# Performance work log

Hardware: AMD Instinct MI355X
Metric: run time of the kernel (lower is better)

Reference implementation:

```python
import jax, jax.numpy as jnp
from jax import lax
import numpy as np

H = 51  # hidden size hardcoded in the module


def setup_inputs() -> dict:
    key = jax.random.key(0)
    ks = jax.random.split(key, 12)
    B, T = 4096, 256
    s_in = 1.0 / np.sqrt(H)
    inp = {
        "input": jax.random.normal(ks[0], (B, T), dtype=jnp.float32),
        # LSTMCell 1: input dim 1 -> hidden 51 (gates stacked i,f,g,o)
        "W_ih1": jax.random.uniform(ks[1], (4 * H, 1), jnp.float32, -s_in, s_in),
        "W_hh1": jax.random.uniform(ks[2], (4 * H, H), jnp.float32, -s_in, s_in),
        "b_ih1": jax.random.uniform(ks[3], (4 * H,), jnp.float32, -s_in, s_in),
        "b_hh1": jax.random.uniform(ks[4], (4 * H,), jnp.float32, -s_in, s_in),
        # LSTMCell 2: hidden 51 -> hidden 51
        "W_ih2": jax.random.uniform(ks[5], (4 * H, H), jnp.float32, -s_in, s_in),
        "W_hh2": jax.random.uniform(ks[6], (4 * H, H), jnp.float32, -s_in, s_in),
        "b_ih2": jax.random.uniform(ks[7], (4 * H,), jnp.float32, -s_in, s_in),
        "b_hh2": jax.random.uniform(ks[8], (4 * H,), jnp.float32, -s_in, s_in),
        # Linear head 51 -> 1
        "W_lin": jax.random.uniform(ks[9], (1, H), jnp.float32, -s_in, s_in),
        "b_lin": jax.random.uniform(ks[10], (1,), jnp.float32, -s_in, s_in),
    }
    return inp


def _lstm_cell(x_t, h, c, W_ih, W_hh, b_ih, b_hh):
    # PyTorch LSTMCell: gates = x W_ih^T + b_ih + h W_hh^T + b_hh, order i,f,g,o
    g = x_t @ W_ih.T + b_ih + h @ W_hh.T + b_hh  # [B, 4H]
    i, f, gg, o = jnp.split(g, 4, axis=-1)
    c_new = jax.nn.sigmoid(f) * c + jax.nn.sigmoid(i) * jnp.tanh(gg)
    h_new = jax.nn.sigmoid(o) * jnp.tanh(c_new)
    return h_new, c_new


def reference(input, W_ih1, W_hh1, b_ih1, b_hh1, W_ih2, W_hh2, b_ih2, b_hh2, W_lin, b_lin):
    B = input.shape[0]
    xs = input.T[:, :, None]  # [T, B, 1] -- one scalar feature per timestep

    def step(carry, x_t):
        h1, c1, h2, c2 = carry
        h1, c1 = _lstm_cell(x_t, h1, c1, W_ih1, W_hh1, b_ih1, b_hh1)
        h2, c2 = _lstm_cell(h1, h2, c2, W_ih2, W_hh2, b_ih2, b_hh2)
        out = h2 @ W_lin.T + b_lin  # [B, 1]
        return (h1, c1, h2, c2), out

    z = jnp.zeros((B, H), dtype=input.dtype)
    _, outs = lax.scan(step, (z, z, z, z), xs)  # outs: [T, B, 1]
    # torch.stack(outputs, 1).squeeze(2) -> [B, T]
    return outs[:, :, 0].T
```

## Files before the change

### kernel.cpp

```cpp
#include <hip/hip_runtime.h>

#define HH 51
#define TT 256
#define NB 16
#define L2E 1.442695041f

typedef __attribute__((ext_vector_type(8))) _Float16 half8;
typedef __attribute__((ext_vector_type(4))) float   floatx4;

#define MFMA16F(A,B,C) __builtin_amdgcn_mfma_f32_16x16x32_f16((A),(B),(C),0,0,0)

__device__ __forceinline__ float rcp_fast(float x) { return __builtin_amdgcn_rcpf(x); }
#if __has_builtin(__builtin_amdgcn_exp2f)
__device__ __forceinline__ float exp2_fast(float x) { return __builtin_amdgcn_exp2f(x); }
#else
__device__ __forceinline__ float exp2_fast(float x) { return __expf(0.69314718056f * x); }
#endif
__device__ __forceinline__ unsigned short f2h_bits(float v) {
    return __builtin_bit_cast(unsigned short, (_Float16)v);
}

__global__ void lstm_prep(const float* __restrict__ Whh1, const float* __restrict__ Wih1,
                          const float* __restrict__ bih1, const float* __restrict__ bhh1,
                          const float* __restrict__ Wih2, const float* __restrict__ Whh2,
                          const float* __restrict__ bih2, const float* __restrict__ bhh2,
                          const float* __restrict__ Wlin, const float* __restrict__ blin,
                          uint4* __restrict__ frags) {
    int tid = blockIdx.x * blockDim.x + threadIdx.x;
    if (tid >= 196 * 64) return;
    int f = tid >> 6, lane = tid & 63;
    int n = lane & 15, qq = lane >> 4;
    int hl, s, tau, cell;
    if (f < 64)       { cell = 1; int r = f;       hl = r & 1; r >>= 1; s = r & 1; tau = r >> 1; }
    else if (f < 192) { cell = 2; int r = f - 64;  hl = r & 1; r >>= 1; s = r & 3; tau = r >> 2; }
    else              { cell = 3; int r = f - 192; hl = r & 1; s = r >> 1; tau = 0; }
    int g = tau >> 2, U = tau & 3, u = U * 16 + n;
    float sc = (cell == 3) ? 1.0f : ((g == 2) ? 2.0f * L2E : L2E);
    unsigned int dw[4];
    for (int d = 0; d < 4; d++) {
        unsigned int packed = 0;
        for (int e = 0; e < 2; e++) {
            int jj = d * 2 + e;
            int k = s * 32 + qq * 8 + jj;
            float val = 0.f;
            if (cell == 1) {
                if (u < HH) {
                    if (k < HH)       val = Whh1[(g * HH + u) * HH + k];
                    else if (k == 51) val = bih1[g * HH + u] + bhh1[g * HH + u];
                    else              val = Wih1[g * HH + u];
                }
            } else if (cell == 2) {
                if (u < HH) {
                    if (k < 64) {
                        if (k < HH)       val = Wih2[(g * HH + u) * HH + k];
                        else if (k == 51) val = bih2[g * HH + u] + bhh2[g * HH + u];
                    } else {
                        int k2 = k - 64;
                        if (k2 < HH) val = Whh2[(g * HH + u) * HH + k2];
                    }
                }
            } else {
                if (n == 0) {
                    if (k < HH)       val = Wlin[k];
                    else if (k == 51) val = blin[0];
                }
            }
            val *= sc;
            _Float16 hi = (_Float16)val;
            unsigned short bits;
            if (hl) { float lo = val - (float)hi; bits = f2h_bits(lo); }
            else    { bits = __builtin_bit_cast(unsigned short, hi); }
            packed |= ((unsigned int)bits) << (16 * e);
        }
        dw[d] = packed;
    }
    frags[f * 64 + lane] = make_uint4(dw[0], dw[1], dw[2], dw[3]);
}

__launch_bounds__(512, 2)
__global__ void lstm_main(const float* __restrict__ input,
                          const uint4* __restrict__ frags,
                          float* __restrict__ out) {
    __shared__ __align__(16) unsigned int h1[2][16][36];
    __shared__ __align__(16) unsigned int h2[2][16][36];
    __shared__ __align__(16) float xb[(TT + 1) * 16];

    const int tid  = threadIdx.x;
    const int lane = tid & 63;
    const int w    = tid >> 6;
    const int l15  = lane & 15;
    const int q    = lane >> 4;
    const int b0g  = blockIdx.x * NB;
    const bool c2w = (w < 4);
    const int U    = c2w ? w : (w - 4);
    const int uc   = U * 16 + l15;
    const bool uok = (uc < HH);

    for (int i = tid; i < 2 * 16 * 36; i += 512) {
        ((unsigned*)h1)[i] = 0; ((unsigned*)h2)[i] = 0;
    }
    for (int c = 0; c < 2; c++) {
        int flat = tid + c * 512;
        int b = flat >> 6, t0 = (flat & 63) * 4;
        float4 v = *(const float4*)&input[(size_t)(b0g + b) * TT + t0];
        xb[(t0 + 0) * 16 + b] = v.x; xb[(t0 + 1) * 16 + b] = v.y;
        xb[(t0 + 2) * 16 + b] = v.z; xb[(t0 + 3) * 16 + b] = v.w;
    }
    if (tid < 16) xb[TT * 16 + tid] = 0.f;
    __syncthreads();
    if (tid < 16) {
        int b = tid;
        int wi51 = ((25 + 4 * (b >> 1)) & 31) * 2 + 1;
        int wi52 = ((26 + 4 * (b >> 1)) & 31) * 2 + 0;
        int wi53 = ((26 + 4 * (b >> 1)) & 31) * 2 + 1;
        ((unsigned short*)&h1[1][b][0])[wi51] = 0x3C00;
        float x0 = input[(size_t)(b0g + b) * TT];
        _Float16 xh = (_Float16)x0;
        ((unsigned short*)&h1[1][b][0])[wi52] = __builtin_bit_cast(unsigned short, xh);
        ((unsigned short*)&h1[1][b][0])[wi53] = f2h_bits(x0 - (float)xh);
    }

    half8 fr[32];
    if (c2w) {
#pragma unroll
        for (int g = 0; g < 4; g++) {
            int tau = g * 4 + U;
#pragma unroll
            for (int s = 0; s < 4; s++) {
                fr[g * 8 + s * 2 + 0] = __builtin_bit_cast(half8, frags[(64 + (tau * 4 + s) * 2 + 0) * 64 + lane]);
                fr[g * 8 + s * 2 + 1] = __builtin_bit_cast(half8, frags[(64 + (tau * 4 + s) * 2 + 1) * 64 + lane]);
            }
        }
    } else {
#pragma unroll
        for (int g = 0; g < 4; g++) {
            int tau = g * 4 + U;
#pragma unroll
            for (int s = 0; s < 2; s++) {
                fr[g * 4 + s * 2 + 0] = __builtin_bit_cast(half8, frags[((tau * 2 + s) * 2 + 0) * 64 + lane]);
                fr[g * 4 + s * 2 + 1] = __builtin_bit_cast(half8, frags[((tau * 2 + s) * 2 + 1) * 64 + lane]);
            }
        }
#pragma unroll
        for (int s = 0; s < 2; s++) {
            fr[16 + s * 2 + 0] = __builtin_bit_cast(half8, frags[(192 + s * 2 + 0) * 64 + lane]);
            fr[16 + s * 2 + 1] = __builtin_bit_cast(half8, frags[(192 + s * 2 + 1) * 64 + lane]);
        }
    }
    floatx4 zacc = {0.f, 0.f, 0.f, 0.f};
    float cst[4] = {0.f, 0.f, 0.f, 0.f};
    const int baseA = (q * 4 + 4 * (l15 >> 1)) & 31;
    const int baseB = (baseA + 16) & 31;

    __syncthreads();

#define GTAIL(DG, FG, SGN)                                                      \
    _Pragma("unroll")                                                           \
    for (int r = 0; r < 4; r++) {                                               \
        float e = exp2_fast(SGN (DG)[r]);                                       \
        (FG)[r] = rcp_fast(1.0f + e);                                           \
    }

#define STEP(IT, P)                                                             \
    do {                                                                        \
        if (c2w) {                                                              \
            if ((IT) >= 1 && (IT) <= TT) {               \
                half8 a0 = *(const half8*)&h1[1 - (P)][l15][baseA];             \
                half8 a1 = *(const half8*)&h1[1 - (P)][l15][baseB];             \
                half8 a2 = *(const half8*)&h2[(P)][l15][baseA];                 \
                half8 a3 = *(const half8*)&h2[(P)][l15][baseB];                 \
                floatx4 d0, d1, d2, d3;                                         \
                d0 = MFMA16F(a0, fr[0],  zacc); d0 = MFMA16F(a0, fr[1],  d0);   \
                d1 = MFMA16F(a0, fr[8],  zacc); d1 = MFMA16F(a0, fr[9],  d1);   \
                d2 = MFMA16F(a0, fr[16], zacc); d2 = MFMA16F(a0, fr[17], d2);   \
                d3 = MFMA16F(a0, fr[24], zacc); d3 = MFMA16F(a0, fr[25], d3);   \
                d0 = MFMA16F(a1, fr[2],  d0);   d0 = MFMA16F(a1, fr[3],  d0);   \
                d1 = MFMA16F(a1, fr[10], d1);   d1 = MFMA16F(a1, fr[11], d1);   \
                d2 = MFMA16F(a1, fr[18], d2);   d2 = MFMA16F(a1, fr[19], d2);   \
                d3 = MFMA16F(a1, fr[26], d3);   d3 = MFMA16F(a1, fr[27], d3);   \
                d0 = MFMA16F(a2, fr[4],  d0);   d0 = MFMA16F(a2, fr[5],  d0);   \
                d1 = MFMA16F(a2, fr[12], d1);   d1 = MFMA16F(a2, fr[13], d1);   \
                d2 = MFMA16F(a2, fr[20], d2);   d2 = MFMA16F(a2, fr[21], d2);   \
                d3 = MFMA16F(a2, fr[28], d3);   d3 = MFMA16F(a2, fr[29], d3);   \
                d0 = MFMA16F(a3, fr[6],  d0);   d0 = MFMA16F(a3, fr[7],  d0);   \
                d1 = MFMA16F(a3, fr[14], d1);   d1 = MFMA16F(a3, fr[15], d1);   \
                d2 = MFMA16F(a3, fr[22], d2);   d2 = MFMA16F(a3, fr[23], d2);   \
                d3 = MFMA16F(a3, fr[30], d3);   d3 = MFMA16F(a3, fr[31], d3);   \
                floatx4 f0, f1, f2, f3;                                         \
                GTAIL(d0, f0, -) GTAIL(d1, f1, -) GTAIL(d2, f2, +) GTAIL(d3, f3, -) \
                _Pragma("unroll")                                               \
                for (int r = 0; r < 4; r++) {                                   \
                    float tgs = fmaf(-4.0f * L2E, f2[r], 2.0f * L2E);           \
                    float cn  = fmaf(f1[r], cst[r], f0[r] * tgs);               \
                    cst[r] = cn;                                                \
                    float th = fmaf(-2.0f, rcp_fast(1.0f + exp2_fast(cn)), 1.0f); \
                    float hv = f3[r] * th;                                      \
                    hv = uok ? hv : (uc == 51 ? 1.0f : 0.f);                    \
                    int bb = q * 4 + r;                                         \
                    int wi = (((uc >> 1) + 4 * (bb >> 1)) & 31) * 2 + (uc & 1); \
                    ((unsigned short*)&h2[1 - (P)][bb][0])[wi] = f2h_bits(hv);  \
                }                                                               \
            }                                                                   \
        } else {                                                                \
            if ((IT) <= TT - 1) {                          \
                float4 xn = {0.f, 0.f, 0.f, 0.f};                               \
                if (uc >= HH) xn = *(const float4*)&xb[((IT) + 1) * 16 + q * 4]; \
                half8 a0 = *(const half8*)&h1[1 - (P)][l15][baseA];             \
                half8 a1 = *(const half8*)&h1[1 - (P)][l15][baseB];             \
                floatx4 d0, d1, d2, d3;                                         \
                d0 = MFMA16F(a0, fr[0],  zacc); d0 = MFMA16F(a0, fr[1],  d0);   \
                d1 = MFMA16F(a0, fr[4],  zacc); d1 = MFMA16F(a0, fr[5],  d1);   \
                d2 = MFMA16F(a0, fr[8],  zacc); d2 = MFMA16F(a0, fr[9],  d2);   \
                d3 = MFMA16F(a0, fr[12], zacc); d3 = MFMA16F(a0, fr[13], d3);   \
                d0 = MFMA16F(a1, fr[2],  d0);   d0 = MFMA16F(a1, fr[3],  d0);   \
                d1 = MFMA16F(a1, fr[6],  d1);   d1 = MFMA16F(a1, fr[7],  d1);   \
                d2 = MFMA16F(a1, fr[10], d2);   d2 = MFMA16F(a1, fr[11], d2);   \
                d3 = MFMA16F(a1, fr[14], d3);   d3 = MFMA16F(a1, fr[15], d3);   \
                floatx4 f0, f1, f2, f3;                                         \
                GTAIL(d0, f0, -) GTAIL(d1, f1, -) GTAIL(d2, f2, +) GTAIL(d3, f3, -) \
                _Pragma("unroll")                                               \
                for (int r = 0; r < 4; r++) {                                   \
                    float tgs = fmaf(-4.0f * L2E, f2[r], 2.0f * L2E);           \
                    float cn  = fmaf(f1[r], cst[r], f0[r] * tgs);               \
                    cst[r] = cn;                                                \
                    float th = fmaf(-2.0f, rcp_fast(1.0f + exp2_fast(cn)), 1.0f); \
                    float hv = f3[r] * th;                                      \
                    hv = uok ? hv                                               \
                             : (uc == 51 ? 1.0f                                 \
                             : (uc == 52 ? xn[r]                                \
                             : (uc == 53 ? xn[r] - (float)(_Float16)xn[r] : 0.f))); \
                    int bb = q * 4 + r;                                         \
                    int wi = (((uc >> 1) + 4 * (bb >> 1)) & 31) * 2 + (uc & 1); \
                    ((unsigned short*)&h1[(P)][bb][0])[wi] = f2h_bits(hv);      \
                }                                                               \
            }                                                                   \
            if ((IT) >= 2 && (w - 4) == ((IT) & 3)) {         \
                half8 a2 = *(const half8*)&h2[(P)][l15][baseA];                 \
                half8 a3 = *(const half8*)&h2[(P)][l15][baseB];                 \
                floatx4 ho;                                                     \
                ho = MFMA16F(a2, fr[16], zacc); ho = MFMA16F(a2, fr[17], ho);   \
                ho = MFMA16F(a3, fr[18], ho);   ho = MFMA16F(a3, fr[19], ho);   \
                if (l15 == 0) {                                                 \
                    _Pragma("unroll")                                           \
                    for (int r = 0; r < 4; r++)                                 \
                        out[(size_t)(b0g + q * 4 + r) * TT + ((IT) - 2)] = ho[r]; \
                }                                                               \
            }                                                                   \
        }                                                                       \
        __syncthreads();                                                        \
    } while (0)

    for (int itp = 0; itp < TT + 2; itp += 2) {
        STEP(itp, 0);
        STEP(itp + 1, 1);
    }
#undef STEP
#undef GTAIL
}

extern "C" void kernel_launch(void* const* d_in, const int* in_sizes, int n_in,
                              void* d_out, int out_size, void* d_ws, size_t ws_size,
                              hipStream_t stream) {
    const float* input = (const float*)d_in[0];
    const float* Wih1  = (const float*)d_in[1];
    const float* Whh1  = (const float*)d_in[2];
    const float* bih1  = (const float*)d_in[3];
    const float* bhh1  = (const float*)d_in[4];
    const float* Wih2  = (const float*)d_in[5];
    const float* Whh2  = (const float*)d_in[6];
    const float* bih2  = (const float*)d_in[7];
    const float* bhh2  = (const float*)d_in[8];
    const float* Wlin  = (const float*)d_in[9];
    const float* blin  = (const float*)d_in[10];

    uint4* frags = (uint4*)d_ws;
    int B = in_sizes[0] / TT;

    lstm_prep<<<49, 256, 0, stream>>>(Whh1, Wih1, bih1, bhh1, Wih2, Whh2,
                                      bih2, bhh2, Wlin, blin, frags);
    lstm_main<<<B / NB, 512, 0, stream>>>(input, frags, (float*)d_out);
}
```

Before: 379.0 us.

## Replace block-wide barriers with LDS counter flags and 4-deep h ring buffers

Replaces the per-step __syncthreads lockstep between layer-1 and layer-2 wavegroups with producer/consumer counters in shared memory, using atomic release/acquire and s_sleep spin-waits. Hidden-state buffers grow from double to quadruple buffering, so layer-1 waves can run up to a few steps ahead of layer-2 waves. The aim is to remove full-workgroup barrier stalls and let the two layers' work overlap. The cost is spin-wait polling overhead, and correctness now rests on the ring depth and the counter targets.

New measurement: 386.8 us. +2.1%, slower.

```diff
diff --git a/kernel.cpp b/kernel.cpp
--- a/kernel.cpp
+++ b/kernel.cpp
@@ -77,13 +77,24 @@
     frags[f * 64 + lane] = make_uint4(dw[0], dw[1], dw[2], dw[3]);
 }
 
+__device__ __forceinline__ void wait_ge(int* c, int tgt) {
+    if (__hip_atomic_load(c, __ATOMIC_ACQUIRE, __HIP_MEMORY_SCOPE_WORKGROUP) >= tgt) return;
+    do { __builtin_amdgcn_s_sleep(1); }
+    while (__hip_atomic_load(c, __ATOMIC_ACQUIRE, __HIP_MEMORY_SCOPE_WORKGROUP) < tgt);
+}
+__device__ __forceinline__ void publish(int* c) {
+    if ((threadIdx.x & 63) == 0)
+        (void)__hip_atomic_fetch_add(c, 1, __ATOMIC_RELEASE, __HIP_MEMORY_SCOPE_WORKGROUP);
+}
+
 __launch_bounds__(512, 2)
 __global__ void lstm_main(const float* __restrict__ input,
                           const uint4* __restrict__ frags,
                           float* __restrict__ out) {
-    __shared__ __align__(16) unsigned int h1[2][16][36];
-    __shared__ __align__(16) unsigned int h2[2][16][36];
+    __shared__ __align__(16) unsigned int h1r[4][16][36];
+    __shared__ __align__(16) unsigned int h2r[4][16][36];
     __shared__ __align__(16) float xb[(TT + 1) * 16];
+    __shared__ int cnt1, cnt2;
 
     const int tid  = threadIdx.x;
     const int lane = tid & 63;
@@ -96,8 +107,8 @@
     const int uc   = U * 16 + l15;
     const bool uok = (uc < HH);
 
-    for (int i = tid; i < 2 * 16 * 36; i += 512) {
-        ((unsigned*)h1)[i] = 0; ((unsigned*)h2)[i] = 0;
+    for (int i = tid; i < 4 * 16 * 36; i += 512) {
+        ((unsigned*)h1r)[i] = 0; ((unsigned*)h2r)[i] = 0;
     }
     for (int c = 0; c < 2; c++) {
         int flat = tid + c * 512;
@@ -107,17 +118,18 @@
         xb[(t0 + 2) * 16 + b] = v.z; xb[(t0 + 3) * 16 + b] = v.w;
     }
     if (tid < 16) xb[TT * 16 + tid] = 0.f;
+    if (tid == 0) { cnt1 = 0; cnt2 = 0; }
     __syncthreads();
     if (tid < 16) {
         int b = tid;
         int wi51 = ((25 + 4 * (b >> 1)) & 31) * 2 + 1;
         int wi52 = ((26 + 4 * (b >> 1)) & 31) * 2 + 0;
         int wi53 = ((26 + 4 * (b >> 1)) & 31) * 2 + 1;
-        ((unsigned short*)&h1[1][b][0])[wi51] = 0x3C00;
+        ((unsigned short*)&h1r[3][b][0])[wi51] = 0x3C00;
         float x0 = input[(size_t)(b0g + b) * TT];
         _Float16 xh = (_Float16)x0;
-        ((unsigned short*)&h1[1][b][0])[wi52] = __builtin_bit_cast(unsigned short, xh);
-        ((unsigned short*)&h1[1][b][0])[wi53] = f2h_bits(x0 - (float)xh);
+        ((unsigned short*)&h1r[3][b][0])[wi52] = __builtin_bit_cast(unsigned short, xh);
+        ((unsigned short*)&h1r[3][b][0])[wi53] = f2h_bits(x0 - (float)xh);
     }
 
     half8 fr[32];
@@ -161,100 +173,102 @@
         (FG)[r] = rcp_fast(1.0f + e);                                           \
     }
 
-#define STEP(IT, P)                                                             \
-    do {                                                                        \
-        if (c2w) {                                                              \
-            if ((IT) >= 1 && (IT) <= TT) {               \
-                half8 a0 = *(const half8*)&h1[1 - (P)][l15][baseA];             \
-                half8 a1 = *(const half8*)&h1[1 - (P)][l15][baseB];             \
-                half8 a2 = *(const half8*)&h2[(P)][l15][baseA];                 \
-                half8 a3 = *(const half8*)&h2[(P)][l15][baseB];                 \
-                floatx4 d0, d1, d2, d3;                                         \
-                d0 = MFMA16F(a0, fr[0],  zacc); d0 = MFMA16F(a0, fr[1],  d0);   \
-                d1 = MFMA16F(a0, fr[8],  zacc); d1 = MFMA16F(a0, fr[9],  d1);   \
-                d2 = MFMA16F(a0, fr[16], zacc); d2 = MFMA16F(a0, fr[17], d2);   \
-                d3 = MFMA16F(a0, fr[24], zacc); d3 = MFMA16F(a0, fr[25], d3);   \
-                d0 = MFMA16F(a1, fr[2],  d0);   d0 = MFMA16F(a1, fr[3],  d0);   \
-                d1 = MFMA16F(a1, fr[10], d1);   d1 = MFMA16F(a1, fr[11], d1);   \
-                d2 = MFMA16F(a1, fr[18], d2);   d2 = MFMA16F(a1, fr[19], d2);   \
-                d3 = MFMA16F(a1, fr[26], d3);   d3 = MFMA16F(a1, fr[27], d3);   \
-                d0 = MFMA16F(a2, fr[4],  d0);   d0 = MFMA16F(a2, fr[5],  d0);   \
-                d1 = MFMA16F(a2, fr[12], d1);   d1 = MFMA16F(a2, fr[13], d1);   \
-                d2 = MFMA16F(a2, fr[20], d2);   d2 = MFMA16F(a2, fr[21], d2);   \
-                d3 = MFMA16F(a2, fr[28], d3);   d3 = MFMA16F(a2, fr[29], d3);   \
-                d0 = MFMA16F(a3, fr[6],  d0);   d0 = MFMA16F(a3, fr[7],  d0);   \
-                d1 = MFMA16F(a3, fr[14], d1);   d1 = MFMA16F(a3, fr[15], d1);   \
-                d2 = MFMA16F(a3, fr[22], d2);   d2 = MFMA16F(a3, fr[23], d2);   \
-                d3 = MFMA16F(a3, fr[30], d3);   d3 = MFMA16F(a3, fr[31], d3);   \
-                floatx4 f0, f1, f2, f3;                                         \
-                GTAIL(d0, f0, -) GTAIL(d1, f1, -) GTAIL(d2, f2, +) GTAIL(d3, f3, -) \
-                _Pragma("unroll")                                               \
-                for (int r = 0; r < 4; r++) {                                   \
-                    float tgs = fmaf(-4.0f * L2E, f2[r], 2.0f * L2E);           \
-                    float cn  = fmaf(f1[r], cst[r], f0[r] * tgs);               \
-                    cst[r] = cn;                                                \
-                    float th = fmaf(-2.0f, rcp_fast(1.0f + exp2_fast(cn)), 1.0f); \
-                    float hv = f3[r] * th;                                      \
-                    hv = uok ? hv : (uc == 51 ? 1.0f : 0.f);                    \
-                    int bb = q * 4 + r;                                         \
-                    int wi = (((uc >> 1) + 4 * (bb >> 1)) & 31) * 2 + (uc & 1); \
-                    ((unsigned short*)&h2[1 - (P)][bb][0])[wi] = f2h_bits(hv);  \
-                }                                                               \
-            }                                                                   \
-        } else {                                                                \
-            if ((IT) <= TT - 1) {                          \
-                float4 xn = {0.f, 0.f, 0.f, 0.f};                               \
-                if (uc >= HH) xn = *(const float4*)&xb[((IT) + 1) * 16 + q * 4]; \
-                half8 a0 = *(const half8*)&h1[1 - (P)][l15][baseA];             \
-                half8 a1 = *(const half8*)&h1[1 - (P)][l15][baseB];             \
-                floatx4 d0, d1, d2, d3;                                         \
-                d0 = MFMA16F(a0, fr[0],  zacc); d0 = MFMA16F(a0, fr[1],  d0);   \
-                d1 = MFMA16F(a0, fr[4],  zacc); d1 = MFMA16F(a0, fr[5],  d1);   \
-                d2 = MFMA16F(a0, fr[8],  zacc); d2 = MFMA16F(a0, fr[9],  d2);   \
-                d3 = MFMA16F(a0, fr[12], zacc); d3 = MFMA16F(a0, fr[13], d3);   \
-                d0 = MFMA16F(a1, fr[2],  d0);   d0 = MFMA16F(a1, fr[3],  d0);   \
-                d1 = MFMA16F(a1, fr[6],  d1);   d1 = MFMA16F(a1, fr[7],  d1);   \
-                d2 = MFMA16F(a1, fr[10], d2);   d2 = MFMA16F(a1, fr[11], d2);   \
-                d3 = MFMA16F(a1, fr[14], d3);   d3 = MFMA16F(a1, fr[15], d3);   \
-                floatx4 f0, f1, f2, f3;                                         \
-                GTAIL(d0, f0, -) GTAIL(d1, f1, -) GTAIL(d2, f2, +) GTAIL(d3, f3, -) \
-                _Pragma("unroll")                                               \
-                for (int r = 0; r < 4; r++) {                                   \
-                    float tgs = fmaf(-4.0f * L2E, f2[r], 2.0f * L2E);           \
-                    float cn  = fmaf(f1[r], cst[r], f0[r] * tgs);               \
-                    cst[r] = cn;                                                \
-                    float th = fmaf(-2.0f, rcp_fast(1.0f + exp2_fast(cn)), 1.0f); \
-                    float hv = f3[r] * th;                                      \
-                    hv = uok ? hv                                               \
-                             : (uc == 51 ? 1.0f                                 \
-                             : (uc == 52 ? xn[r]                                \
-                             : (uc == 53 ? xn[r] - (float)(_Float16)xn[r] : 0.f))); \
-                    int bb = q * 4 + r;                                         \
-                    int wi = (((uc >> 1) + 4 * (bb >> 1)) & 31) * 2 + (uc & 1); \
-                    ((unsigned short*)&h1[(P)][bb][0])[wi] = f2h_bits(hv);      \
-                }                                                               \
-            }                                                                   \
-            if ((IT) >= 2 && (w - 4) == ((IT) & 3)) {         \
-                half8 a2 = *(const half8*)&h2[(P)][l15][baseA];                 \
-                half8 a3 = *(const half8*)&h2[(P)][l15][baseB];                 \
-                floatx4 ho;                                                     \
-                ho = MFMA16F(a2, fr[16], zacc); ho = MFMA16F(a2, fr[17], ho);   \
-                ho = MFMA16F(a3, fr[18], ho);   ho = MFMA16F(a3, fr[19], ho);   \
-                if (l15 == 0) {                                                 \
-                    _Pragma("unroll")                                           \
-                    for (int r = 0; r < 4; r++)                                 \
-                        out[(size_t)(b0g + q * 4 + r) * TT + ((IT) - 2)] = ho[r]; \
-                }                                                               \
-            }                                                                   \
-        }                                                                       \
-        __syncthreads();                                                        \
-    } while (0)
-
-    for (int itp = 0; itp < TT + 2; itp += 2) {
-        STEP(itp, 0);
-        STEP(itp + 1, 1);
-    }
-#undef STEP
+    if (c2w) {
+        for (int s = 0; s < TT; ++s) {
+            wait_ge(&cnt2, 4 * s);
+            wait_ge(&cnt1, 4 * (s + 1));
+            const unsigned int* p1 = &h1r[s & 3][l15][0];
+            const unsigned int* p2 = &h2r[(s + 3) & 3][l15][0];
+            half8 a0 = *(const half8*)(p1 + baseA);
+            half8 a1 = *(const half8*)(p1 + baseB);
+            half8 a2 = *(const half8*)(p2 + baseA);
+            half8 a3 = *(const half8*)(p2 + baseB);
+            floatx4 d0, d1, d2, d3;
+            d0 = MFMA16F(a0, fr[0],  zacc); d0 = MFMA16F(a0, fr[1],  d0);
+            d1 = MFMA16F(a0, fr[8],  zacc); d1 = MFMA16F(a0, fr[9],  d1);
+            d2 = MFMA16F(a0, fr[16], zacc); d2 = MFMA16F(a0, fr[17], d2);
+            d3 = MFMA16F(a0, fr[24], zacc); d3 = MFMA16F(a0, fr[25], d3);
+            d0 = MFMA16F(a1, fr[2],  d0);   d0 = MFMA16F(a1, fr[3],  d0);
+            d1 = MFMA16F(a1, fr[10], d1);   d1 = MFMA16F(a1, fr[11], d1);
+            d2 = MFMA16F(a1, fr[18], d2);   d2 = MFMA16F(a1, fr[19], d2);
+            d3 = MFMA16F(a1, fr[26], d3);   d3 = MFMA16F(a1, fr[27], d3);
+            d0 = MFMA16F(a2, fr[4],  d0);   d0 = MFMA16F(a2, fr[5],  d0);
+            d1 = MFMA16F(a2, fr[12], d1);   d1 = MFMA16F(a2, fr[13], d1);
+            d2 = MFMA16F(a2, fr[20], d2);   d2 = MFMA16F(a2, fr[21], d2);
+            d3 = MFMA16F(a2, fr[28], d3);   d3 = MFMA16F(a2, fr[29], d3);
+            d0 = MFMA16F(a3, fr[6],  d0);   d0 = MFMA16F(a3, fr[7],  d0);
+            d1 = MFMA16F(a3, fr[14], d1);   d1 = MFMA16F(a3, fr[15], d1);
+            d2 = MFMA16F(a3, fr[22], d2);   d2 = MFMA16F(a3, fr[23], d2);
+            d3 = MFMA16F(a3, fr[30], d3);   d3 = MFMA16F(a3, fr[31], d3);
+            floatx4 f0, f1, f2, f3;
+            GTAIL(d0, f0, -) GTAIL(d1, f1, -) GTAIL(d2, f2, +) GTAIL(d3, f3, -)
+#pragma unroll
+            for (int r = 0; r < 4; r++) {
+                float tgs = fmaf(-4.0f * L2E, f2[r], 2.0f * L2E);
+                float cn  = fmaf(f1[r], cst[r], f0[r] * tgs);
+                cst[r] = cn;
+                float th = fmaf(-2.0f, rcp_fast(1.0f + exp2_fast(cn)), 1.0f);
+                float hv = f3[r] * th;
+                hv = uok ? hv : (uc == 51 ? 1.0f : 0.f);
+                int bb = q * 4 + r;
+                int wi = (((uc >> 1) + 4 * (bb >> 1)) & 31) * 2 + (uc & 1);
+                ((unsigned short*)&h2r[s & 3][bb][0])[wi] = f2h_bits(hv);
+            }
+            publish(&cnt2);
+        }
+    } else {
+        for (int t = 0; t < TT + 4; ++t) {
+            wait_ge(&cnt1, 4 * t);
+            if (t >= 4) wait_ge(&cnt2, 4 * (t - 3));
+            if (t >= 4 && U == (t & 3)) {
+                const unsigned int* p2 = &h2r[t & 3][l15][0];
+                half8 a2 = *(const half8*)(p2 + baseA);
+                half8 a3 = *(const half8*)(p2 + baseB);
+                floatx4 ho;
+                ho = MFMA16F(a2, fr[16], zacc); ho = MFMA16F(a2, fr[17], ho);
+                ho = MFMA16F(a3, fr[18], ho);   ho = MFMA16F(a3, fr[19], ho);
+                if (l15 == 0) {
+#pragma unroll
+                    for (int r = 0; r < 4; r++)
+                        out[(size_t)(b0g + q * 4 + r) * TT + (t - 4)] = ho[r];
+                }
+            }
+            if (t < TT) {
+                float4 xn = {0.f, 0.f, 0.f, 0.f};
+                if (uc >= HH) xn = *(const float4*)&xb[(t + 1) * 16 + q * 4];
+                const unsigned int* p1 = &h1r[(t + 3) & 3][l15][0];
+                half8 a0 = *(const half8*)(p1 + baseA);
+                half8 a1 = *(const half8*)(p1 + baseB);
+                floatx4 d0, d1, d2, d3;
+                d0 = MFMA16F(a0, fr[0],  zacc); d0 = MFMA16F(a0, fr[1],  d0);
+                d1 = MFMA16F(a0, fr[4],  zacc); d1 = MFMA16F(a0, fr[5],  d1);
+                d2 = MFMA16F(a0, fr[8],  zacc); d2 = MFMA16F(a0, fr[9],  d2);
+                d3 = MFMA16F(a0, fr[12], zacc); d3 = MFMA16F(a0, fr[13], d3);
+                d0 = MFMA16F(a1, fr[2],  d0);   d0 = MFMA16F(a1, fr[3],  d0);
+                d1 = MFMA16F(a1, fr[6],  d1);   d1 = MFMA16F(a1, fr[7],  d1);
+                d2 = MFMA16F(a1, fr[10], d2);   d2 = MFMA16F(a1, fr[11], d2);
+                d3 = MFMA16F(a1, fr[14], d3);   d3 = MFMA16F(a1, fr[15], d3);
+                floatx4 f0, f1, f2, f3;
+                GTAIL(d0, f0, -) GTAIL(d1, f1, -) GTAIL(d2, f2, +) GTAIL(d3, f3, -)
+#pragma unroll
+                for (int r = 0; r < 4; r++) {
+                    float tgs = fmaf(-4.0f * L2E, f2[r], 2.0f * L2E);
+                    float cn  = fmaf(f1[r], cst[r], f0[r] * tgs);
+                    cst[r] = cn;
+                    float th = fmaf(-2.0f, rcp_fast(1.0f + exp2_fast(cn)), 1.0f);
+                    float hv = f3[r] * th;
+                    hv = uok ? hv
+                             : (uc == 51 ? 1.0f
+                             : (uc == 52 ? xn[r]
+                             : (uc == 53 ? xn[r] - (float)(_Float16)xn[r] : 0.f)));
+                    int bb = q * 4 + r;
+                    int wi = (((uc >> 1) + 4 * (bb >> 1)) & 31) * 2 + (uc & 1);
+                    ((unsigned short*)&h1r[t & 3][bb][0])[wi] = f2h_bits(hv);
+                }
+            }
+            publish(&cnt1);
+        }
+    }
 #undef GTAIL
 }
 
```

## Merge cell1 and cell2 wave roles so each wave computes both layers

Applied to the files above, without the earlier changes.

The block shrinks from 8 waves, where 4 handled layer 1 and 4 handled layer 2 plus the output head, to 4 waves. Each wave now computes its slice of both LSTM cells and the linear head every step, and holds all weight fragments in registers. The aim is to fill the MFMA pipeline and reuse the shared-memory h1 loads across both cells, cutting per-step barrier cost and idle waves. In exchange, each wave holds more registers (52 half8 fragments) and does about twice the serial work per step, with fewer waves per CU to hide latency.

After: 466.2 us. 23.0% more time.

```diff
diff --git a/kernel.cpp b/kernel.cpp
--- a/kernel.cpp
+++ b/kernel.cpp
@@ -77,7 +77,7 @@
     frags[f * 64 + lane] = make_uint4(dw[0], dw[1], dw[2], dw[3]);
 }
 
-__launch_bounds__(512, 2)
+__launch_bounds__(256, 1)
 __global__ void lstm_main(const float* __restrict__ input,
                           const uint4* __restrict__ frags,
                           float* __restrict__ out) {
@@ -91,16 +91,14 @@
     const int l15  = lane & 15;
     const int q    = lane >> 4;
     const int b0g  = blockIdx.x * NB;
-    const bool c2w = (w < 4);
-    const int U    = c2w ? w : (w - 4);
-    const int uc   = U * 16 + l15;
+    const int uc   = w * 16 + l15;
     const bool uok = (uc < HH);
 
-    for (int i = tid; i < 2 * 16 * 36; i += 512) {
+    for (int i = tid; i < 2 * 16 * 36; i += 256) {
         ((unsigned*)h1)[i] = 0; ((unsigned*)h2)[i] = 0;
     }
-    for (int c = 0; c < 2; c++) {
-        int flat = tid + c * 512;
+    for (int c = 0; c < 4; c++) {
+        int flat = tid + c * 256;
         int b = flat >> 6, t0 = (flat & 63) * 4;
         float4 v = *(const float4*)&input[(size_t)(b0g + b) * TT + t0];
         xb[(t0 + 0) * 16 + b] = v.x; xb[(t0 + 1) * 16 + b] = v.y;
@@ -120,35 +118,30 @@
         ((unsigned short*)&h1[1][b][0])[wi53] = f2h_bits(x0 - (float)xh);
     }
 
-    half8 fr[32];
-    if (c2w) {
-#pragma unroll
-        for (int g = 0; g < 4; g++) {
-            int tau = g * 4 + U;
-#pragma unroll
-            for (int s = 0; s < 4; s++) {
-                fr[g * 8 + s * 2 + 0] = __builtin_bit_cast(half8, frags[(64 + (tau * 4 + s) * 2 + 0) * 64 + lane]);
-                fr[g * 8 + s * 2 + 1] = __builtin_bit_cast(half8, frags[(64 + (tau * 4 + s) * 2 + 1) * 64 + lane]);
-            }
+    half8 fr1[16], fr2[32], frh[4];
+#pragma unroll
+    for (int g = 0; g < 4; g++) {
+        int tau = g * 4 + w;
+#pragma unroll
+        for (int s = 0; s < 2; s++) {
+            fr1[g * 4 + s * 2 + 0] = __builtin_bit_cast(half8, frags[((tau * 2 + s) * 2 + 0) * 64 + lane]);
+            fr1[g * 4 + s * 2 + 1] = __builtin_bit_cast(half8, frags[((tau * 2 + s) * 2 + 1) * 64 + lane]);
         }
-    } else {
-#pragma unroll
-        for (int g = 0; g < 4; g++) {
-            int tau = g * 4 + U;
-#pragma unroll
-            for (int s = 0; s < 2; s++) {
-                fr[g * 4 + s * 2 + 0] = __builtin_bit_cast(half8, frags[((tau * 2 + s) * 2 + 0) * 64 + lane]);
-                fr[g * 4 + s * 2 + 1] = __builtin_bit_cast(half8, frags[((tau * 2 + s) * 2 + 1) * 64 + lane]);
-            }
+#pragma unroll
+        for (int s = 0; s < 4; s++) {
+            fr2[g * 8 + s * 2 + 0] = __builtin_bit_cast(half8, frags[(64 + (tau * 4 + s) * 2 + 0) * 64 + lane]);
+            fr2[g * 8 + s * 2 + 1] = __builtin_bit_cast(half8, frags[(64 + (tau * 4 + s) * 2 + 1) * 64 + lane]);
         }
-#pragma unroll
-        for (int s = 0; s < 2; s++) {
-            fr[16 + s * 2 + 0] = __builtin_bit_cast(half8, frags[(192 + s * 2 + 0) * 64 + lane]);
-            fr[16 + s * 2 + 1] = __builtin_bit_cast(half8, frags[(192 + s * 2 + 1) * 64 + lane]);
-        }
-    }
+    }
+#pragma unroll
+    for (int s = 0; s < 2; s++) {
+        frh[s * 2 + 0] = __builtin_bit_cast(half8, frags[(192 + s * 2 + 0) * 64 + lane]);
+        frh[s * 2 + 1] = __builtin_bit_cast(half8, frags[(192 + s * 2 + 1) * 64 + lane]);
+    }
+
     floatx4 zacc = {0.f, 0.f, 0.f, 0.f};
-    float cst[4] = {0.f, 0.f, 0.f, 0.f};
+    float cst1[4] = {0.f, 0.f, 0.f, 0.f};
+    float cst2[4] = {0.f, 0.f, 0.f, 0.f};
     const int baseA = (q * 4 + 4 * (l15 >> 1)) & 31;
     const int baseB = (baseA + 16) & 31;
 
@@ -161,100 +154,105 @@
         (FG)[r] = rcp_fast(1.0f + e);                                           \
     }
 
-#define STEP(IT, P)                                                             \
+#define ITER(N, P)                                                              \
     do {                                                                        \
-        if (c2w) {                                                              \
-            if ((IT) >= 1 && (IT) <= TT) {               \
-                half8 a0 = *(const half8*)&h1[1 - (P)][l15][baseA];             \
-                half8 a1 = *(const half8*)&h1[1 - (P)][l15][baseB];             \
-                half8 a2 = *(const half8*)&h2[(P)][l15][baseA];                 \
-                half8 a3 = *(const half8*)&h2[(P)][l15][baseB];                 \
-                floatx4 d0, d1, d2, d3;                                         \
-                d0 = MFMA16F(a0, fr[0],  zacc); d0 = MFMA16F(a0, fr[1],  d0);   \
-                d1 = MFMA16F(a0, fr[8],  zacc); d1 = MFMA16F(a0, fr[9],  d1);   \
-                d2 = MFMA16F(a0, fr[16], zacc); d2 = MFMA16F(a0, fr[17], d2);   \
-                d3 = MFMA16F(a0, fr[24], zacc); d3 = MFMA16F(a0, fr[25], d3);   \
-                d0 = MFMA16F(a1, fr[2],  d0);   d0 = MFMA16F(a1, fr[3],  d0);   \
-                d1 = MFMA16F(a1, fr[10], d1);   d1 = MFMA16F(a1, fr[11], d1);   \
-                d2 = MFMA16F(a1, fr[18], d2);   d2 = MFMA16F(a1, fr[19], d2);   \
-                d3 = MFMA16F(a1, fr[26], d3);   d3 = MFMA16F(a1, fr[27], d3);   \
-                d0 = MFMA16F(a2, fr[4],  d0);   d0 = MFMA16F(a2, fr[5],  d0);   \
-                d1 = MFMA16F(a2, fr[12], d1);   d1 = MFMA16F(a2, fr[13], d1);   \
-                d2 = MFMA16F(a2, fr[20], d2);   d2 = MFMA16F(a2, fr[21], d2);   \
-                d3 = MFMA16F(a2, fr[28], d3);   d3 = MFMA16F(a2, fr[29], d3);   \
-                d0 = MFMA16F(a3, fr[6],  d0);   d0 = MFMA16F(a3, fr[7],  d0);   \
-                d1 = MFMA16F(a3, fr[14], d1);   d1 = MFMA16F(a3, fr[15], d1);   \
-                d2 = MFMA16F(a3, fr[22], d2);   d2 = MFMA16F(a3, fr[23], d2);   \
-                d3 = MFMA16F(a3, fr[30], d3);   d3 = MFMA16F(a3, fr[31], d3);   \
-                floatx4 f0, f1, f2, f3;                                         \
-                GTAIL(d0, f0, -) GTAIL(d1, f1, -) GTAIL(d2, f2, +) GTAIL(d3, f3, -) \
-                _Pragma("unroll")                                               \
-                for (int r = 0; r < 4; r++) {                                   \
-                    float tgs = fmaf(-4.0f * L2E, f2[r], 2.0f * L2E);           \
-                    float cn  = fmaf(f1[r], cst[r], f0[r] * tgs);               \
-                    cst[r] = cn;                                                \
-                    float th = fmaf(-2.0f, rcp_fast(1.0f + exp2_fast(cn)), 1.0f); \
-                    float hv = f3[r] * th;                                      \
-                    hv = uok ? hv : (uc == 51 ? 1.0f : 0.f);                    \
-                    int bb = q * 4 + r;                                         \
-                    int wi = (((uc >> 1) + 4 * (bb >> 1)) & 31) * 2 + (uc & 1); \
-                    ((unsigned short*)&h2[1 - (P)][bb][0])[wi] = f2h_bits(hv);  \
-                }                                                               \
+        const bool do1 = (N) < TT;                                              \
+        const bool do2 = ((N) >= 1) && ((N) <= TT);                             \
+        const bool doH = ((N) >= 2) && ((N) <= TT + 1) && (w == ((N) & 3));     \
+        const unsigned int* p1r = &h1[1 - (P)][l15][0];            \
+        half8 a0 = *(const half8*)(p1r + baseA);                                \
+        half8 a1 = *(const half8*)(p1r + baseB);                                \
+        half8 a2, a3;                                                           \
+        if ((N) >= 1) {                                                         \
+            const unsigned int* p2r = &h2[(P)][l15][0];            \
+            a2 = *(const half8*)(p2r + baseA);                                  \
+            a3 = *(const half8*)(p2r + baseB);                                  \
+        }                                                                       \
+        floatx4 d0, d1, d2, d3;                                                 \
+        if (do1) {                                   \
+            d0 = MFMA16F(a0, fr1[0],  zacc); d0 = MFMA16F(a0, fr1[1],  d0);     \
+            d1 = MFMA16F(a0, fr1[4],  zacc); d1 = MFMA16F(a0, fr1[5],  d1);     \
+            d2 = MFMA16F(a0, fr1[8],  zacc); d2 = MFMA16F(a0, fr1[9],  d2);     \
+            d3 = MFMA16F(a0, fr1[12], zacc); d3 = MFMA16F(a0, fr1[13], d3);     \
+            d0 = MFMA16F(a1, fr1[2],  d0);   d0 = MFMA16F(a1, fr1[3],  d0);     \
+            d1 = MFMA16F(a1, fr1[6],  d1);   d1 = MFMA16F(a1, fr1[7],  d1);     \
+            d2 = MFMA16F(a1, fr1[10], d2);   d2 = MFMA16F(a1, fr1[11], d2);     \
+            d3 = MFMA16F(a1, fr1[14], d3);   d3 = MFMA16F(a1, fr1[15], d3);     \
+        }                                                                       \
+        floatx4 e0, e1, e2, e3, ho;                                             \
+        if (do2) {                                   \
+            e0 = MFMA16F(a0, fr2[0],  zacc); e0 = MFMA16F(a0, fr2[1],  e0);     \
+            e1 = MFMA16F(a0, fr2[8],  zacc); e1 = MFMA16F(a0, fr2[9],  e1);     \
+            e2 = MFMA16F(a0, fr2[16], zacc); e2 = MFMA16F(a0, fr2[17], e2);     \
+            e3 = MFMA16F(a0, fr2[24], zacc); e3 = MFMA16F(a0, fr2[25], e3);     \
+            e0 = MFMA16F(a1, fr2[2],  e0);   e0 = MFMA16F(a1, fr2[3],  e0);     \
+            e1 = MFMA16F(a1, fr2[10], e1);   e1 = MFMA16F(a1, fr2[11], e1);     \
+            e2 = MFMA16F(a1, fr2[18], e2);   e2 = MFMA16F(a1, fr2[19], e2);     \
+            e3 = MFMA16F(a1, fr2[26], e3);   e3 = MFMA16F(a1, fr2[27], e3);     \
+            e0 = MFMA16F(a2, fr2[4],  e0);   e0 = MFMA16F(a2, fr2[5],  e0);     \
+            e1 = MFMA16F(a2, fr2[12], e1);   e1 = MFMA16F(a2, fr2[13], e1);     \
+            e2 = MFMA16F(a2, fr2[20], e2);   e2 = MFMA16F(a2, fr2[21], e2);     \
+            e3 = MFMA16F(a2, fr2[28], e3);   e3 = MFMA16F(a2, fr2[29], e3);     \
+            e0 = MFMA16F(a3, fr2[6],  e0);   e0 = MFMA16F(a3, fr2[7],  e0);     \
+            e1 = MFMA16F(a3, fr2[14], e1);   e1 = MFMA16F(a3, fr2[15], e1);     \
+            e2 = MFMA16F(a3, fr2[22], e2);   e2 = MFMA16F(a3, fr2[23], e2);     \
+            e3 = MFMA16F(a3, fr2[30], e3);   e3 = MFMA16F(a3, fr2[31], e3);     \
+        }                                                                       \
+        if (doH) {                               \
+            ho = MFMA16F(a2, frh[0], zacc); ho = MFMA16F(a2, frh[1], ho);       \
+            ho = MFMA16F(a3, frh[2], ho);   ho = MFMA16F(a3, frh[3], ho);       \
+        }                                                                       \
+        if (do1) {                                     \
+            float4 xn = {0.f, 0.f, 0.f, 0.f};                                   \
+            if (uc >= HH) xn = *(const float4*)&xb[((N) + 1) * 16 + q * 4];     \
+            floatx4 f0, f1, f2, f3;                                             \
+            GTAIL(d0, f0, -) GTAIL(d1, f1, -) GTAIL(d2, f2, +) GTAIL(d3, f3, -) \
+            _Pragma("unroll")                                                   \
+            for (int r = 0; r < 4; r++) {                                       \
+                float tgs = fmaf(-4.0f * L2E, f2[r], 2.0f * L2E);               \
+                float cn  = fmaf(f1[r], cst1[r], f0[r] * tgs);                  \
+                cst1[r] = cn;                                                   \
+                float th = fmaf(-2.0f, rcp_fast(1.0f + exp2_fast(cn)), 1.0f);   \
+                float hv = f3[r] * th;                                          \
+                hv = uok ? hv                                                   \
+                         : (uc == 51 ? 1.0f                                     \
+                         : (uc == 52 ? xn[r]                                    \
+                         : (uc == 53 ? xn[r] - (float)(_Float16)xn[r] : 0.f))); \
+                int bb = q * 4 + r;                                             \
+                int wi = (((uc >> 1) + 4 * (bb >> 1)) & 31) * 2 + (uc & 1);     \
+                ((unsigned short*)&h1[(P)][bb][0])[wi] = f2h_bits(hv);          \
             }                                                                   \
-        } else {                                                                \
-            if ((IT) <= TT - 1) {                          \
-                float4 xn = {0.f, 0.f, 0.f, 0.f};                               \
-                if (uc >= HH) xn = *(const float4*)&xb[((IT) + 1) * 16 + q * 4]; \
-                half8 a0 = *(const half8*)&h1[1 - (P)][l15][baseA];             \
-                half8 a1 = *(const half8*)&h1[1 - (P)][l15][baseB];             \
-                floatx4 d0, d1, d2, d3;                                         \
-                d0 = MFMA16F(a0, fr[0],  zacc); d0 = MFMA16F(a0, fr[1],  d0);   \
-                d1 = MFMA16F(a0, fr[4],  zacc); d1 = MFMA16F(a0, fr[5],  d1);   \
-                d2 = MFMA16F(a0, fr[8],  zacc); d2 = MFMA16F(a0, fr[9],  d2);   \
-                d3 = MFMA16F(a0, fr[12], zacc); d3 = MFMA16F(a0, fr[13], d3);   \
-                d0 = MFMA16F(a1, fr[2],  d0);   d0 = MFMA16F(a1, fr[3],  d0);   \
-                d1 = MFMA16F(a1, fr[6],  d1);   d1 = MFMA16F(a1, fr[7],  d1);   \
-                d2 = MFMA16F(a1, fr[10], d2);   d2 = MFMA16F(a1, fr[11], d2);   \
-                d3 = MFMA16F(a1, fr[14], d3);   d3 = MFMA16F(a1, fr[15], d3);   \
-                floatx4 f0, f1, f2, f3;                                         \
-                GTAIL(d0, f0, -) GTAIL(d1, f1, -) GTAIL(d2, f2, +) GTAIL(d3, f3, -) \
-                _Pragma("unroll")                                               \
-                for (int r = 0; r < 4; r++) {                                   \
-                    float tgs = fmaf(-4.0f * L2E, f2[r], 2.0f * L2E);           \
-                    float cn  = fmaf(f1[r], cst[r], f0[r] * tgs);               \
-                    cst[r] = cn;                                                \
-                    float th = fmaf(-2.0f, rcp_fast(1.0f + exp2_fast(cn)), 1.0f); \
-                    float hv = f3[r] * th;                                      \
-                    hv = uok ? hv                                               \
-                             : (uc == 51 ? 1.0f                                 \
-                             : (uc == 52 ? xn[r]                                \
-                             : (uc == 53 ? xn[r] - (float)(_Float16)xn[r] : 0.f))); \
-                    int bb = q * 4 + r;                                         \
-                    int wi = (((uc >> 1) + 4 * (bb >> 1)) & 31) * 2 + (uc & 1); \
-                    ((unsigned short*)&h1[(P)][bb][0])[wi] = f2h_bits(hv);      \
-                }                                                               \
+        }                                                                       \
+        if (do2) {                                   \
+            floatx4 f0, f1, f2, f3;                                             \
+            GTAIL(e0, f0, -) GTAIL(e1, f1, -) GTAIL(e2, f2, +) GTAIL(e3, f3, -) \
+            _Pragma("unroll")                                                   \
+            for (int r = 0; r < 4; r++) {                                       \
+                float tgs = fmaf(-4.0f * L2E, f2[r], 2.0f * L2E);               \
+                float cn  = fmaf(f1[r], cst2[r], f0[r] * tgs);                  \
+                cst2[r] = cn;                                                   \
+                float th = fmaf(-2.0f, rcp_fast(1.0f + exp2_fast(cn)), 1.0f);   \
+                float hv = f3[r] * th;                                          \
+                hv = uok ? hv : (uc == 51 ? 1.0f : 0.f);                        \
+                int bb = q * 4 + r;                                             \
+                int wi = (((uc >> 1) + 4 * (bb >> 1)) & 31) * 2 + (uc & 1);     \
+                ((unsigned short*)&h2[1 - (P)][bb][0])[wi] = f2h_bits(hv);      \
             }                                                                   \
-            if ((IT) >= 2 && (w - 4) == ((IT) & 3)) {         \
-                half8 a2 = *(const half8*)&h2[(P)][l15][baseA];                 \
-                half8 a3 = *(const half8*)&h2[(P)][l15][baseB];                 \
-                floatx4 ho;                                                     \
-                ho = MFMA16F(a2, fr[16], zacc); ho = MFMA16F(a2, fr[17], ho);   \
-                ho = MFMA16F(a3, fr[18], ho);   ho = MFMA16F(a3, fr[19], ho);   \
-                if (l15 == 0) {                                                 \
-                    _Pragma("unroll")                                           \
-                    for (int r = 0; r < 4; r++)                                 \
-                        out[(size_t)(b0g + q * 4 + r) * TT + ((IT) - 2)] = ho[r]; \
-                }                                                               \
-            }                                                                   \
+        }                                                                       \
+        if (doH && l15 == 0) {                                                  \
+            _Pragma("unroll")                                                   \
+            for (int r = 0; r < 4; r++)                                         \
+                out[(size_t)(b0g + q * 4 + r) * TT + ((N) - 2)] = ho[r];        \
         }                                                                       \
         __syncthreads();                                                        \
     } while (0)
 
-    for (int itp = 0; itp < TT + 2; itp += 2) {
-        STEP(itp, 0);
-        STEP(itp + 1, 1);
-    }
-#undef STEP
+#pragma unroll 1
+    for (int n0 = 0; n0 < TT + 2; n0 += 2) {
+        ITER(n0, 0);
+        ITER(n0 + 1, 1);
+    }
+#undef ITER
 #undef GTAIL
 }
 
@@ -278,5 +276,5 @@
 
     lstm_prep<<<49, 256, 0, stream>>>(Whh1, Wih1, bih1, bhh1, Wih2, Whh2,
                                       bih2, bhh2, Wlin, blin, frags);
-    lstm_main<<<B / NB, 512, 0, stream>>>(input, frags, (float*)d_out);
-}
+    lstm_main<<<B / NB, 256, 0, stream>>>(input, frags, (float*)d_out);
+}
```
